# Kernel tuning notes

Hardware: AMD Instinct MI355X
Metric: run time of the kernel (lower is better)

The kernel has to match this reference:

```python
import jax, jax.numpy as jnp
from jax import lax
import numpy as np

N, T, U = 8, 300, 60
E_ENC, E_DEC, NHID, VOCAB, BLANK = 320, 320, 512, 128, 0


def setup_inputs() -> dict:
    key = jax.random.key(0)
    ks = jax.random.split(key, 6)
    enc_state = jax.random.normal(ks[0], (N, T, E_ENC), jnp.float32)
    dec_state = jax.random.normal(ks[1], (N, U + 1, E_DEC), jnp.float32)
    targets = jax.random.randint(ks[2], (N, U), 1, VOCAB, jnp.int32)  # non-blank labels
    inputs_len = jnp.full((N,), T, jnp.int32)
    targets_len = jnp.full((N,), U, jnp.int32)
    W_joint = jax.random.normal(ks[3], (E_ENC + E_DEC, NHID), jnp.float32) * (1.0 / np.sqrt(E_ENC + E_DEC))
    b_joint = jnp.zeros((NHID,), jnp.float32)
    W_out = jax.random.normal(ks[4], (NHID, VOCAB), jnp.float32) * (1.0 / np.sqrt(NHID))
    b_out = jnp.zeros((VOCAB,), jnp.float32)
    return dict(enc_state=enc_state, dec_state=dec_state, targets=targets,
                inputs_len=inputs_len, targets_len=targets_len,
                W_joint=W_joint, b_joint=b_joint, W_out=W_out, b_out=b_out)


def _joint_log_probs(enc, dec, Wj, bj, Wo, bo):
    # Original: broadcast enc [N,T,1,Ee] + dec [N,1,U1,Ed], concat, Linear, Tanh, Linear, log_softmax.
    # Splitting W_joint over the concat axis is exactly equivalent and avoids the [N,T,U1,Ee+Ed] tensor.
    Ee = enc.shape[-1]
    h = (jnp.einsum('nte,eh->nth', enc, Wj[:Ee])[:, :, None, :]
         + jnp.einsum('nue,eh->nuh', dec, Wj[Ee:])[:, None, :, :]
         + bj)                                              # [N,T,U1,NHID]
    logits = jnp.einsum('ntuh,hv->ntuv', jnp.tanh(h), Wo) + bo  # [N,T,U1,V]
    return jax.nn.log_softmax(logits, axis=-1)


def _rnnt_loss(logp, targets, inputs_len, targets_len, blank):
    # Forward (alpha) DP over the T x (U+1) lattice, vectorized over batch.
    Nb, Tt, U1, V = logp.shape
    blank_lp = logp[..., blank]                                        # [N,T,U1]
    emit_lp = jnp.take_along_axis(logp[:, :, :U1 - 1, :],
                                  targets[:, None, :, None], axis=-1)[..., 0]  # [N,T,U]
    # Row t=0: alpha[0,u] = sum_{u'<u} emit[0,u'].
    a0 = jnp.concatenate([jnp.zeros((Nb, 1), logp.dtype),
                          jnp.cumsum(emit_lp[:, 0, :], axis=1)], axis=1)       # [N,U1]

    def row_step(prev, xs):
        blank_tm1, emit_t = xs                      # [N,U1], [N,U]
        base = prev + blank_tm1                     # path arriving from (t-1,u) via blank

        def u_step(carry, xs_u):
            b_u, e_u = xs_u                         # [N], [N]
            v = jnp.logaddexp(b_u, carry + e_u)     # blank-from-below vs emit-from-left
            return v, v

        _, rest = lax.scan(u_step, base[:, 0], (base[:, 1:].T, emit_t.T))      # [U,N]
        row = jnp.concatenate([base[:, :1], rest.T], axis=1)                   # [N,U1]
        return row, row

    _, rows = lax.scan(row_step, a0,
                       (jnp.swapaxes(blank_lp[:, :-1], 0, 1),
                        jnp.swapaxes(emit_lp[:, 1:], 0, 1)))                   # [T-1,N,U1]
    alpha = jnp.concatenate([a0[:, None, :], jnp.swapaxes(rows, 0, 1)], axis=1)  # [N,T,U1]

    ti = (inputs_len - 1).astype(jnp.int32)
    ui = targets_len.astype(jnp.int32)
    n = jnp.arange(Nb)
    log_p = alpha[n, ti, ui] + blank_lp[n, ti, ui]  # final blank transition
    return -log_p


def reference(enc_state, dec_state, targets, inputs_len, targets_len,
              W_joint, b_joint, W_out, b_out):
    logp = _joint_log_probs(enc_state, dec_state, W_joint, b_joint, W_out, b_out)
    loss = _rnnt_loss(logp, targets, inputs_len, targets_len, BLANK)
    return loss.mean()
```

## Files before the change

### kernel.cpp

```cpp
#include <hip/hip_runtime.h>
#include <hip/hip_bf16.h>
#include <hip/hip_fp16.h>

#define N_   8
#define T_   300
#define U_   60
#define U1_  61
#define EENC 320
#define NHID 512
#define VOC  128
#define SKROWS 384
#define INV_LN2 1.4426950408889634f
#define LN2 0.6931471805599453f
#define SCALE2 2.8853900817779268f

typedef __attribute__((ext_vector_type(8))) short bf16x8;
typedef __attribute__((ext_vector_type(4))) float f32x4;

__device__ __forceinline__ unsigned short f2bf(float f) {
    unsigned int u = __float_as_uint(f);
    u += 0x7fff + ((u >> 16) & 1);
    return (unsigned short)(u >> 16);
}

__device__ __forceinline__ float lae2(float x, float y) {
    float m = fmaxf(x, y);
    float d = fminf(fabsf(x - y), 1e30f);
    return m + log2f(1.f + exp2f(-d));
}

__device__ __forceinline__ float4 gload16(const void* p) {
    float4 v;
    asm volatile("global_load_dwordx4 %0, %1, off" : "=v"(v) : "v"(p) : "memory");
    return v;
}
#define WAITVM(n) __builtin_amdgcn_s_waitcnt(0x0F70 | (n))

__global__ __launch_bounds__(256) void convert_w(
    const float* __restrict__ Wj, const float* __restrict__ Wo,
    unsigned short* __restrict__ WjT, unsigned short* __restrict__ WoT2,
    float* __restrict__ bosum)
{
    __shared__ float tile[32][33];
    int bid = blockIdx.x;
    const float* S; unsigned short* D; int k0, c0, K, C; bool isWo;
    if (bid < 160) { S = Wj; D = WjT; K = 320; C = 512; k0 = (bid >> 4) * 32; c0 = (bid & 15) * 32; isWo = false; }
    else { bid -= 160; S = Wo; D = WoT2; K = 512; C = 128; k0 = (bid >> 2) * 32; c0 = (bid & 3) * 32; isWo = true; }
    const int tx = threadIdx.x & 31, ty = threadIdx.x >> 5;
    float part = 0.f;
    #pragma unroll
    for (int i = 0; i < 32; i += 8) {
        float v = S[(k0 + ty + i) * C + c0 + tx];
        tile[ty + i][tx] = v;
        part += v;
    }
    __syncthreads();
    const float mulf = isWo ? -2.f : 1.f;
    #pragma unroll
    for (int i = 0; i < 32; i += 8)
        D[(c0 + ty + i) * K + k0 + tx] = f2bf(mulf * tile[tx][ty + i]);
    if (isWo) atomicAdd(&bosum[c0 + tx], part);
}

__global__ __launch_bounds__(256) void proj_mfma(
    const float* __restrict__ Xe, const float* __restrict__ Xd,
    const unsigned short* __restrict__ BT,
    const float* __restrict__ bj,
    float* __restrict__ Ce, float* __restrict__ Cd)
{
    __shared__ short lA[64 * 64];
    __shared__ short lB[128 * 64];
    int bid = blockIdx.x;
    const float* X; float* Cp; const float* bias; int R;
    if (bid < 152) { X = Xe; Cp = Ce; bias = nullptr; R = N_ * T_; }
    else { bid -= 152; X = Xd; Cp = Cd; bias = bj; R = N_ * U1_; }
    const int tid = threadIdx.x, lane = tid & 63, wave = tid >> 6;
    const int rb = bid >> 2, cb = bid & 3;
    const int rh = wave & 1, ch = wave >> 1;
    const int sr = tid >> 3, sg = tid & 7;
    const int frow = lane & 15, fg = lane >> 4, quad = lane >> 4;

    f32x4 acc[2][4];
    f32x4 z = {0.f, 0.f, 0.f, 0.f};
    #pragma unroll
    for (int a = 0; a < 2; ++a)
        #pragma unroll
        for (int b = 0; b < 4; ++b) acc[a][b] = z;

    for (int s = 0; s < 5; ++s) {
        __syncthreads();
        #pragma unroll
        for (int p = 0; p < 2; ++p) {
            int row = sr + p * 32;
            int grow = rb * 64 + row; if (grow >= R) grow = R - 1;
            const float* xp = X + grow * EENC + s * 64 + sg * 8;
            float4 x0 = *(const float4*)xp, x1 = *(const float4*)(xp + 4);
            bf16x8 va;
            va[0] = (short)f2bf(x0.x); va[1] = (short)f2bf(x0.y);
            va[2] = (short)f2bf(x0.z); va[3] = (short)f2bf(x0.w);
            va[4] = (short)f2bf(x1.x); va[5] = (short)f2bf(x1.y);
            va[6] = (short)f2bf(x1.z); va[7] = (short)f2bf(x1.w);
            *(bf16x8*)&lA[row * 64 + ((sg ^ (row & 7)) << 3)] = va;
        }
        #pragma unroll
        for (int p = 0; p < 4; ++p) {
            int col = sr + p * 32;
            bf16x8 vb = *(const bf16x8*)(BT + (cb * 128 + col) * EENC + s * 64 + sg * 8);
            *(bf16x8*)&lB[col * 64 + ((sg ^ (col & 7)) << 3)] = vb;
        }
        __syncthreads();
        #pragma unroll
        for (int ks = 0; ks < 2; ++ks) {
            int g = fg + ks * 4;
            bf16x8 af[2], bf[4];
            #pragma unroll
            for (int rt = 0; rt < 2; ++rt) {
                int row = rh * 32 + rt * 16 + frow;
                af[rt] = *(const bf16x8*)&lA[row * 64 + ((g ^ (row & 7)) << 3)];
            }
            #pragma unroll
            for (int c = 0; c < 4; ++c) {
                int col = ch * 64 + c * 16 + frow;
                bf[c] = *(const bf16x8*)&lB[col * 64 + ((g ^ (col & 7)) << 3)];
            }
            #pragma unroll
            for (int rt = 0; rt < 2; ++rt)
                #pragma unroll
                for (int c = 0; c < 4; ++c)
                    acc[rt][c] = __builtin_amdgcn_mfma_f32_16x16x32_bf16(af[rt], bf[c], acc[rt][c], 0, 0, 0);
        }
    }
    #pragma unroll
    for (int rt = 0; rt < 2; ++rt) {
        int grow0 = rb * 64 + rh * 32 + rt * 16 + quad * 4;
        #pragma unroll
        for (int c = 0; c < 4; ++c) {
            int col = cb * 128 + ch * 64 + c * 16 + frow;
            float b = bias ? bias[col] : 0.f;
            #pragma unroll
            for (int r = 0; r < 4; ++r) {
                int gr = grow0 + r;
                if (gr < R) Cp[gr * NHID + col] = (acc[rt][c][r] + b) * SCALE2;
            }
        }
    }
}

__global__ __launch_bounds__(512, 4) void joint_mfma(
    const float* __restrict__ encp,
    const float* __restrict__ decp,
    const unsigned short* __restrict__ WoT2,
    const float* __restrict__ bo, const float* __restrict__ bosum,
    const int* __restrict__ targets,
    unsigned short* __restrict__ Zs)
{
    __shared__ short lA[256 * 64];
    __shared__ short lB[128 * 64];
    __shared__ float bo_s[VOC];
    __shared__ int   lab_s[U_];

    const int tid = threadIdx.x, lane = tid & 63, wave = tid >> 6;
    const int nt0 = 4 * blockIdx.x, n = nt0 / T_;
    const int t0 = nt0 - n * T_;
    if (tid < VOC) bo_s[tid] = bo[tid] + bosum[tid];
    else if (tid < VOC + U_) lab_s[tid - VOC] = targets[n * U_ + (tid - VOC)];

    const int frow = lane & 15, quad = lane >> 4;
    const int sg = tid & 7, sr = tid >> 3;

    f32x4 acc[2][8];
    f32x4 z = {0.f, 0.f, 0.f, 0.f};
    #pragma unroll
    for (int rt = 0; rt < 2; ++rt)
        #pragma unroll
        for (int c = 0; c < 8; ++c) acc[rt][c] = z;

    const int ua = min(sr, U_);
    const float* dbase = decp + (size_t)(n * U1_ + ua) * NHID + sg * 8;
    const float* ebase = encp + (size_t)nt0 * NHID + sg * 8;

    for (int s = 0; s < 8; ++s) {
        __syncthreads();
        #pragma unroll
        for (int p = 0; p < 2; ++p) {
            int col = sr + p * 64;
            bf16x8 vb = *(const bf16x8*)(WoT2 + col * NHID + s * 64 + sg * 8);
            *(bf16x8*)&lB[col * 64 + ((sg ^ (col & 7)) << 3)] = vb;
        }
        const float* dp = dbase + s * 64;
        float4 d0 = *(const float4*)dp, d1 = *(const float4*)(dp + 4);
        #pragma unroll
        for (int p = 0; p < 4; ++p) {
            const float* ep = ebase + (size_t)p * NHID + s * 64;
            float4 e0 = *(const float4*)ep, e1 = *(const float4*)(ep + 4);
            float s0 = __builtin_amdgcn_rcpf(__builtin_amdgcn_exp2f(e0.x + d0.x) + 1.f);
            float s1 = __builtin_amdgcn_rcpf(__builtin_amdgcn_exp2f(e0.y + d0.y) + 1.f);
            float s2 = __builtin_amdgcn_rcpf(__builtin_amdgcn_exp2f(e0.z + d0.z) + 1.f);
            float s3 = __builtin_amdgcn_rcpf(__builtin_amdgcn_exp2f(e0.w + d0.w) + 1.f);
            float s4 = __builtin_amdgcn_rcpf(__builtin_amdgcn_exp2f(e1.x + d1.x) + 1.f);
            float s5 = __builtin_amdgcn_rcpf(__builtin_amdgcn_exp2f(e1.y + d1.y) + 1.f);
            float s6 = __builtin_amdgcn_rcpf(__builtin_amdgcn_exp2f(e1.z + d1.z) + 1.f);
            float s7 = __builtin_amdgcn_rcpf(__builtin_amdgcn_exp2f(e1.w + d1.w) + 1.f);
            unsigned b0 = __float_as_uint(s0) + 0x8000u, b1 = __float_as_uint(s1) + 0x8000u;
            unsigned b2 = __float_as_uint(s2) + 0x8000u, b3 = __float_as_uint(s3) + 0x8000u;
            unsigned b4 = __float_as_uint(s4) + 0x8000u, b5 = __float_as_uint(s5) + 0x8000u;
            unsigned b6 = __float_as_uint(s6) + 0x8000u, b7 = __float_as_uint(s7) + 0x8000u;
            union { unsigned u4[4]; bf16x8 v; } va;
            va.u4[0] = __builtin_amdgcn_perm(b1, b0, 0x07060302);
            va.u4[1] = __builtin_amdgcn_perm(b3, b2, 0x07060302);
            va.u4[2] = __builtin_amdgcn_perm(b5, b4, 0x07060302);
            va.u4[3] = __builtin_amdgcn_perm(b7, b6, 0x07060302);
            int row = sr + p * 64;
            *(bf16x8*)&lA[row * 64 + ((sg ^ (row & 7)) << 3)] = va.v;
        }
        __syncthreads();
        #pragma unroll
        for (int ks = 0; ks < 2; ++ks) {
            const int g = ks * 4 + quad;
            bf16x8 af[2];
            #pragma unroll
            for (int rt = 0; rt < 2; ++rt) {
                int ar = wave * 32 + rt * 16 + frow;
                af[rt] = *(const bf16x8*)&lA[ar * 64 + ((g ^ (ar & 7)) << 3)];
            }
            #pragma unroll
            for (int c = 0; c < 8; ++c) {
                int col = c * 16 + frow;
                const bf16x8 bfr = *(const bf16x8*)&lB[col * 64 + ((g ^ (col & 7)) << 3)];
                acc[0][c] = __builtin_amdgcn_mfma_f32_16x16x32_bf16(af[0], bfr, acc[0][c], 0, 0, 0);
                acc[1][c] = __builtin_amdgcn_mfma_f32_16x16x32_bf16(af[1], bfr, acc[1][c], 0, 0, 0);
            }
        }
    }

    #pragma unroll
    for (int rt = 0; rt < 2; ++rt) {
        #pragma unroll
        for (int c = 0; c < 8; ++c) {
            float b = bo_s[c * 16 + frow];
            #pragma unroll
            for (int r = 0; r < 4; ++r) acc[rt][c][r] += b;
        }
        float mx[4], sm[4];
        #pragma unroll
        for (int r = 0; r < 4; ++r) {
            float m = acc[rt][0][r];
            #pragma unroll
            for (int c = 1; c < 8; ++c) m = fmaxf(m, acc[rt][c][r]);
            mx[r] = m;
        }
        #pragma unroll
        for (int off = 1; off < 16; off <<= 1)
            #pragma unroll
            for (int r = 0; r < 4; ++r) mx[r] = fmaxf(mx[r], __shfl_xor(mx[r], off));
        #pragma unroll
        for (int r = 0; r < 4; ++r) {
            float ss = 0.f;
            #pragma unroll
            for (int c = 0; c < 8; ++c) ss += __expf(acc[rt][c][r] - mx[r]);
            sm[r] = ss;
        }
        #pragma unroll
        for (int off = 1; off < 16; off <<= 1)
            #pragma unroll
            for (int r = 0; r < 4; ++r) sm[r] += __shfl_xor(sm[r], off);

        #pragma unroll
        for (int r = 0; r < 4; ++r) {
            float lse = mx[r] + __logf(sm[r]);
            int row = wave * 32 + rt * 16 + quad * 4 + r;
            int urow = row & 63, ntl = row >> 6;
            size_t rowz = (size_t)(n * SKROWS + t0 + ntl + urow + 1) * 64;
            if (urow < U1_ && frow == 0) {
                __half hh = __float2half_rn((acc[rt][0][r] - lse) * INV_LN2);
                Zs[(rowz + urow) * 2] = __half_as_ushort(hh);
            }
            if (urow < U_) {
                int lab = lab_s[urow];
                if (frow == (lab & 15)) {
                    int cw = lab >> 4;
                    float pick = acc[rt][0][r];
                    #pragma unroll
                    for (int c = 1; c < 8; ++c) if (c == cw) pick = acc[rt][c][r];
                    __half hh = __float2half_rn((pick - lse) * INV_LN2);
                    Zs[(rowz + urow + 1) * 2 + 1] = __half_as_ushort(hh);
                }
            }
        }
    }
}

__global__ __launch_bounds__(128) void dp_kernel(
    const unsigned* __restrict__ Z,
    const int* __restrict__ inputs_len, const int* __restrict__ targets_len,
    float* __restrict__ out)
{
    __shared__ float losses[N_];
    const int tid = threadIdx.x;
    const int n  = tid >> 4;
    const int c  = tid & 15;
    const int u0 = c * 4;
    const char* Zn = (const char*)(Z + (size_t)n * SKROWS * 64) + u0 * 4;
    const unsigned len_t = (unsigned)inputs_len[n];
    const int ui = targets_len[n];
    const int ti = (int)len_t - 1;
    const bool u_is0 = (c == 0);

    float a0 = u_is0 ? 0.f : -1e30f;
    float a1 = -1e30f, a2 = -1e30f, a3 = -1e30f;

    float4 zq[8];
    #pragma unroll
    for (int j = 0; j < 8; ++j) zq[j] = gload16(Zn + (size_t)(1 + j) * 256);

    for (int d0 = 1; d0 < 361; d0 += 8) {
        #pragma unroll
        for (int j = 0; j < 8; ++j) {
            const int d = d0 + j;
            WAITVM(7);
            float4 zv = zq[j];
            zq[j] = gload16(Zn + (size_t)(d + 8) * 256);
            const __half2* hz = (const __half2*)&zv;
            float2 w0 = __half22float2(hz[0]);
            float2 w1 = __half22float2(hz[1]);
            float2 w2 = __half22float2(hz[2]);
            float2 w3 = __half22float2(hz[3]);
            float av0 = __shfl_up(a3, 1);
            float e0 = u_is0 ? -1e30f : w0.y;
            float n0 = lae2(a0 + w0.x, av0 + e0);
            float n1 = lae2(a1 + w1.x, a0 + w1.y);
            float n2 = lae2(a2 + w2.x, a1 + w2.y);
            float n3 = lae2(a3 + w3.x, a2 + w3.y);
            a0 = ((unsigned)(d - u0)     < len_t) ? n0 : a0;
            a1 = ((unsigned)(d - u0 - 1) < len_t) ? n1 : a1;
            a2 = ((unsigned)(d - u0 - 2) < len_t) ? n2 : a2;
            a3 = ((unsigned)(d - u0 - 3) < len_t) ? n3 : a3;
        }
    }
    WAITVM(0);
    float av[4] = {a0, a1, a2, a3};
    #pragma unroll
    for (int j = 0; j < 4; ++j)
        if (u0 + j == ui) {
            const __half2* hf = (const __half2*)((const char*)(Z + (size_t)n * SKROWS * 64)
                                                 + ((size_t)(ti + ui + 1) * 64 + ui) * 4);
            float blf = __half22float2(hf[0]).x;
            losses[n] = -(av[j] + blf) * LN2;
        }
    __syncthreads();
    if (tid == 0) {
        float s = 0.f;
        #pragma unroll
        for (int i = 0; i < N_; ++i) s += losses[i];
        out[0] = s * (1.0f / N_);
    }
}

extern "C" void kernel_launch(void* const* d_in, const int* in_sizes, int n_in,
                              void* d_out, int out_size, void* d_ws, size_t ws_size,
                              hipStream_t stream)
{
    const float* enc         = (const float*)d_in[0];
    const float* dec         = (const float*)d_in[1];
    const int*   targets     = (const int*)d_in[2];
    const int*   inputs_len  = (const int*)d_in[3];
    const int*   targets_len = (const int*)d_in[4];
    const float* Wj          = (const float*)d_in[5];
    const float* bj          = (const float*)d_in[6];
    const float* Wo          = (const float*)d_in[7];
    const float* bo          = (const float*)d_in[8];
    float* out = (float*)d_out;

    char* ws = (char*)d_ws;
    float*          encp  = (float*)(ws + 0);
    float*          decp  = (float*)(ws + 4915200);
    unsigned*       Z     = (unsigned*)(ws + 5914624);
    unsigned short* WjT   = (unsigned short*)(ws + 6701056);
    unsigned short* WoT2  = (unsigned short*)(ws + 7028736);
    float*          bosum = (float*)(ws + 7159872);

    hipMemsetAsync(bosum, 0, VOC * sizeof(float), stream);
    convert_w<<<224, 256, 0, stream>>>(Wj, Wo, WjT, WoT2, bosum);
    proj_mfma<<<184, 256, 0, stream>>>(enc, dec, WjT, bj, encp, decp);
    joint_mfma<<<600, 512, 0, stream>>>(encp, decp, WoT2, bo, bosum, targets, (unsigned short*)Z);
    dp_kernel<<<1, 128, 0, stream>>>(Z, inputs_len, targets_len, out);
}
```

Before: 214.8 us.

## Stage per-batch DP lattice in LDS with one block per sequence

The DP kernel now launches one block per batch element. Each block first bulk-copies that sequence's skewed log-prob lattice from global memory into shared memory, and then 16 lanes run the anti-diagonal recurrence reading from LDS instead of through a software-prefetched global load queue. The final mean is done with atomicAdd into an output zeroed by the weight-conversion kernel, and the shuffle is reordered to shorten the dependency chain. The aim is to take global-memory latency off the serial DP loop, at the cost of an up-front copy and a barrier.

```diff
diff --git a/kernel.cpp b/kernel.cpp
--- a/kernel.cpp
+++ b/kernel.cpp
@@ -10,6 +10,7 @@
 #define NHID 512
 #define VOC  128
 #define SKROWS 384
+#define ZROWS  361
 #define INV_LN2 1.4426950408889634f
 #define LN2 0.6931471805599453f
 #define SCALE2 2.8853900817779268f
@@ -29,20 +30,14 @@
     return m + log2f(1.f + exp2f(-d));
 }
 
-__device__ __forceinline__ float4 gload16(const void* p) {
-    float4 v;
-    asm volatile("global_load_dwordx4 %0, %1, off" : "=v"(v) : "v"(p) : "memory");
-    return v;
-}
-#define WAITVM(n) __builtin_amdgcn_s_waitcnt(0x0F70 | (n))
-
 __global__ __launch_bounds__(256) void convert_w(
     const float* __restrict__ Wj, const float* __restrict__ Wo,
     unsigned short* __restrict__ WjT, unsigned short* __restrict__ WoT2,
-    float* __restrict__ bosum)
+    float* __restrict__ bosum, float* __restrict__ outz)
 {
     __shared__ float tile[32][33];
     int bid = blockIdx.x;
+    if (bid == 0 && threadIdx.x == 0) outz[0] = 0.f;
     const float* S; unsigned short* D; int k0, c0, K, C; bool isWo;
     if (bid < 160) { S = Wj; D = WjT; K = 320; C = 512; k0 = (bid >> 4) * 32; c0 = (bid & 15) * 32; isWo = false; }
     else { bid -= 160; S = Wo; D = WoT2; K = 512; C = 128; k0 = (bid >> 2) * 32; c0 = (bid & 3) * 32; isWo = true; }
@@ -290,17 +285,22 @@
     }
 }
 
-__global__ __launch_bounds__(128) void dp_kernel(
+__global__ __launch_bounds__(512) void dp_kernel(
     const unsigned* __restrict__ Z,
     const int* __restrict__ inputs_len, const int* __restrict__ targets_len,
     float* __restrict__ out)
 {
-    __shared__ float losses[N_];
+    __shared__ unsigned lz[ZROWS * 64];
     const int tid = threadIdx.x;
-    const int n  = tid >> 4;
-    const int c  = tid & 15;
-    const int u0 = c * 4;
-    const char* Zn = (const char*)(Z + (size_t)n * SKROWS * 64) + u0 * 4;
+    const int n = blockIdx.x;
+    const uint4* src = (const uint4*)(Z + (size_t)n * SKROWS * 64);
+    const int total4 = ZROWS * 16;
+    for (int i = tid; i < total4; i += 512)
+        *(uint4*)&lz[i * 4] = src[i];
+    __syncthreads();
+    if (tid >= 16) return;
+
+    const int c = tid, u0 = c * 4;
     const unsigned len_t = (unsigned)inputs_len[n];
     const int ui = targets_len[n];
     const int ti = (int)len_t - 1;
@@ -308,52 +308,40 @@
 
     float a0 = u_is0 ? 0.f : -1e30f;
     float a1 = -1e30f, a2 = -1e30f, a3 = -1e30f;
-
-    float4 zq[8];
-    #pragma unroll
-    for (int j = 0; j < 8; ++j) zq[j] = gload16(Zn + (size_t)(1 + j) * 256);
+    float av0 = __shfl_up(a3, 1);
 
     for (int d0 = 1; d0 < 361; d0 += 8) {
         #pragma unroll
         for (int j = 0; j < 8; ++j) {
             const int d = d0 + j;
-            WAITVM(7);
-            float4 zv = zq[j];
-            zq[j] = gload16(Zn + (size_t)(d + 8) * 256);
+            uint4 zv = *(const uint4*)&lz[d * 64 + u0];
             const __half2* hz = (const __half2*)&zv;
             float2 w0 = __half22float2(hz[0]);
             float2 w1 = __half22float2(hz[1]);
             float2 w2 = __half22float2(hz[2]);
             float2 w3 = __half22float2(hz[3]);
-            float av0 = __shfl_up(a3, 1);
             float e0 = u_is0 ? -1e30f : w0.y;
+            float n3 = lae2(a3 + w3.x, a2 + w3.y);
+            float n2 = lae2(a2 + w2.x, a1 + w2.y);
+            float n1 = lae2(a1 + w1.x, a0 + w1.y);
+            a3 = ((unsigned)(d - u0 - 3) < len_t) ? n3 : a3;
             float n0 = lae2(a0 + w0.x, av0 + e0);
-            float n1 = lae2(a1 + w1.x, a0 + w1.y);
-            float n2 = lae2(a2 + w2.x, a1 + w2.y);
-            float n3 = lae2(a3 + w3.x, a2 + w3.y);
+            a2 = ((unsigned)(d - u0 - 2) < len_t) ? n2 : a2;
+            a1 = ((unsigned)(d - u0 - 1) < len_t) ? n1 : a1;
             a0 = ((unsigned)(d - u0)     < len_t) ? n0 : a0;
-            a1 = ((unsigned)(d - u0 - 1) < len_t) ? n1 : a1;
-            a2 = ((unsigned)(d - u0 - 2) < len_t) ? n2 : a2;
-            a3 = ((unsigned)(d - u0 - 3) < len_t) ? n3 : a3;
-        }
-    }
-    WAITVM(0);
+            av0 = __shfl_up(a3, 1);
+        }
+    }
+
     float av[4] = {a0, a1, a2, a3};
     #pragma unroll
     for (int j = 0; j < 4; ++j)
         if (u0 + j == ui) {
-            const __half2* hf = (const __half2*)((const char*)(Z + (size_t)n * SKROWS * 64)
-                                                 + ((size_t)(ti + ui + 1) * 64 + ui) * 4);
-            float blf = __half22float2(hf[0]).x;
-            losses[n] = -(av[j] + blf) * LN2;
-        }
-    __syncthreads();
-    if (tid == 0) {
-        float s = 0.f;
-        #pragma unroll
-        for (int i = 0; i < N_; ++i) s += losses[i];
-        out[0] = s * (1.0f / N_);
-    }
+            unsigned wbl = lz[(ti + ui + 1) * 64 + ui];
+            __half2 hv = *(__half2*)&wbl;
+            float blf = __half22float2(hv).x;
+            atomicAdd(out, -(av[j] + blf) * (LN2 / N_));
+        }
 }
 
 extern "C" void kernel_launch(void* const* d_in, const int* in_sizes, int n_in,
@@ -380,8 +368,8 @@
     float*          bosum = (float*)(ws + 7159872);
 
     hipMemsetAsync(bosum, 0, VOC * sizeof(float), stream);
-    convert_w<<<224, 256, 0, stream>>>(Wj, Wo, WjT, WoT2, bosum);
+    convert_w<<<224, 256, 0, stream>>>(Wj, Wo, WjT, WoT2, bosum, out);
     proj_mfma<<<184, 256, 0, stream>>>(enc, dec, WjT, bj, encp, decp);
     joint_mfma<<<600, 512, 0, stream>>>(encp, decp, WoT2, bo, bosum, targets, (unsigned short*)Z);
-    dp_kernel<<<1, 128, 0, stream>>>(Z, inputs_len, targets_len, out);
-}
+    dp_kernel<<<N_, 512, 0, stream>>>(Z, inputs_len, targets_len, out);
+}
```

Result: slower. 238.3 us (+10.9%).
